# Optimization experiments

Hardware: AMD Instinct MI355X
Metric: run time of the kernel (lower is better)

The kernel has to match this reference:

```python
import jax, jax.numpy as jnp
import numpy as np

TAU = 0.07          # softmax temperature
THR = 0.3           # Jaccard similarity threshold for positive pairs
EPS_NORM = 1e-12    # F.normalize eps


def setup_inputs() -> dict:
    key = jax.random.key(0)
    k1, k2, k3 = jax.random.split(key, 3)
    N, D, A = 4096, 128, 512
    z1 = jax.random.normal(k1, (N, D), dtype=jnp.float32)
    z2 = jax.random.normal(k2, (N, D), dtype=jnp.float32)
    labels = jax.random.randint(k3, (N, A), 0, 2).astype(jnp.int32)
    return {"z1": z1, "z2": z2, "labels": labels}


def _l2_normalize(x):
    n = jnp.linalg.norm(x, axis=-1, keepdims=True)
    return x / jnp.maximum(n, EPS_NORM)


def reference(z1, z2, labels):
    # Implements the N > 1000 (chunked) branch of SupConLoss.forward,
    # vectorized over all anchors at once (chunking is just tiling; math identical).
    N = z1.shape[0]
    idx = jnp.arange(N)

    z1n = _l2_normalize(z1)                       # (N, D)
    z2n = _l2_normalize(z2)                       # (N, D)
    z_all = jnp.concatenate([z1n, z2n], axis=0)   # (2N, D)

    # Jaccard label similarity -> positive-pair mask
    lab = labels.astype(jnp.float32)              # (N, A)
    inter = lab @ lab.T                           # (N, N)
    s = lab.sum(axis=1, keepdims=True)            # (N, 1)
    union = s + s.T - inter
    jaccard = inter / (union + 1e-8)
    pos_label = jaccard >= THR                    # (N, N) bool

    # pos mask over 2N columns: label-positives in both halves,
    # augmented view [j, N+j] forced True, self column [j, j] forced False.
    pos_mask = jnp.concatenate([pos_label, pos_label], axis=1)  # (N, 2N)
    pos_mask = pos_mask.at[idx, N + idx].set(True)
    pos_mask = pos_mask.at[idx, idx].set(False)

    # similarity of z1 anchors against all 2N embeddings
    sim = (z1n @ z_all.T) / TAU                   # (N, 2N)
    sim = sim - jax.lax.stop_gradient(sim.max(axis=1, keepdims=True))
    exp_sim = jnp.exp(sim)

    # denominator excludes the self column [j, j]
    denom = exp_sim.sum(axis=1, keepdims=True) - exp_sim[idx, idx][:, None]
    log_prob = sim - jnp.log(denom + 1e-8)

    num_pos = jnp.maximum(pos_mask.sum(axis=1), 1)
    loss_per_sample = -jnp.where(pos_mask, log_prob, 0.0).sum(axis=1) / num_pos
    return loss_per_sample.sum() / N
```

## Files before the change

### kernel.cpp

```cpp
#include <hip/hip_runtime.h>
#include <math.h>

#define N_ROWS 4096
#define DIM    128
#define A_LAB  512
#define INV_TAU 14.285714285714286f

typedef __attribute__((ext_vector_type(8))) short short8;
typedef __attribute__((ext_vector_type(4))) float f32x4;
typedef __attribute__((ext_vector_type(4))) int i32x4;
typedef __attribute__((ext_vector_type(16))) int i32x16;


__device__ __forceinline__ unsigned short f2bf(float f) {
  unsigned int u = __builtin_bit_cast(unsigned int, f);
  u += 0x7fffu + ((u >> 16) & 1u);
  return (unsigned short)(u >> 16);
}

__device__ __forceinline__ void gl_lds16(const void* g, void* l) {
  __builtin_amdgcn_global_load_lds(
      (const __attribute__((address_space(1))) unsigned int*)g,
      (__attribute__((address_space(3))) unsigned int*)l, 16, 0, 0);
}

__global__ __launch_bounds__(256) void k_norm_pack(
    const float* __restrict__ z1, const float* __restrict__ z2,
    const int* __restrict__ labels,
    unsigned int* __restrict__ zbf, uint2* __restrict__ labs8,
    int* __restrict__ s, float* __restrict__ part, float* __restrict__ out)
{
  {
    const int idx = blockIdx.x * 256 + threadIdx.x;
    if (idx < 3 * 4096) part[idx] = 0.0f;
    if (idx == 0) out[0] = 0.0f;
  }
  const int wave = threadIdx.x >> 6, lane = threadIdx.x & 63;
  const int r = blockIdx.x * 4 + wave;
  const float* src = (r < N_ROWS) ? (z1 + (size_t)r * DIM)
                                  : (z2 + (size_t)(r - N_ROWS) * DIM);
  float2 x = ((const float2*)src)[lane];
  float ss = x.x * x.x + x.y * x.y;
  #pragma unroll
  for (int off = 32; off > 0; off >>= 1) ss += __shfl_xor(ss, off);
  const float inv = 1.0f / fmaxf(sqrtf(ss), 1e-12f);
  const unsigned int lo = f2bf(x.x * inv);
  const unsigned int hi = f2bf(x.y * inv);
  {
    const int U  = lane >> 2;
    const int Up = U ^ (r & 15);
    zbf[(size_t)r * 64 + Up * 4 + (lane & 3)] = (hi << 16) | lo;
  }

  if (r < N_ROWS) {
    const int4* lp = (const int4*)(labels + (size_t)r * A_LAB);
    const int4 a = lp[2 * lane], b = lp[2 * lane + 1];
    const unsigned int w0 = (unsigned int)(a.x != 0)       | ((unsigned int)(a.y != 0) << 8)
                          | ((unsigned int)(a.z != 0) << 16) | ((unsigned int)(a.w != 0) << 24);
    const unsigned int w1 = (unsigned int)(b.x != 0)       | ((unsigned int)(b.y != 0) << 8)
                          | ((unsigned int)(b.z != 0) << 16) | ((unsigned int)(b.w != 0) << 24);
    uint2 v; v.x = w0; v.y = w1;
    const int Ul  = lane >> 1;
    const int cc  = Ul >> 3, uu = Ul & 7;
    const int Ulp = (cc << 3) | (uu ^ (r & 7));
    labs8[(size_t)r * 64 + Ulp * 2 + (lane & 1)] = v;
    int cnt = __popc(w0) + __popc(w1);
    #pragma unroll
    for (int off = 32; off > 0; off >>= 1) cnt += __shfl_xor(cnt, off);
    if (lane == 0) s[r] = cnt;
  }
}

__global__ __launch_bounds__(256, 2) void k_fused(
    const unsigned char* __restrict__ labs8, const int* __restrict__ s,
    const unsigned short* __restrict__ zbf, float* __restrict__ part)
{
  __shared__ uint4 lds[4096];
  __shared__ unsigned int pmL[128 * 4];
  const int tid = threadIdx.x;
  const int ibase = blockIdx.x * 128, jbase = blockIdx.y * 128;
  const int wave = tid >> 6, lane = tid & 63;

  const int jwr = (wave >> 1) * 64, jwc = (wave & 1) * 64;
  const int col32 = lane & 31, h = lane >> 5;

  const int s3i = 3 * s[ibase + jwr + lane];
  const int s3j = 3 * s[jbase + jwc + lane];

  #pragma unroll
  for (int it = 0; it < 4; ++it) {
    const int g = wave * 256 + it * 64 + lane;
    const int r = g >> 3, u = g & 7;
    gl_lds16(labs8 + (((size_t)(ibase + r)) << 9) + u * 16,
             &lds[wave * 256 + it * 64]);
    gl_lds16(labs8 + (((size_t)(jbase + r)) << 9) + u * 16,
             &lds[1024 + wave * 256 + it * 64]);
  }
  __syncthreads();

  i32x16 jacc[2][2];
  #pragma unroll
  for (int rt = 0; rt < 2; ++rt)
    #pragma unroll
    for (int nt = 0; nt < 2; ++nt)
      #pragma unroll
      for (int e = 0; e < 16; ++e) jacc[rt][nt][e] = 0;

  for (int ck = 0; ck < 4; ++ck) {
    const int cur = (ck & 1) * 2048;
    if (ck < 3) {
      const int nxt = ((ck + 1) & 1) * 2048;
      #pragma unroll
      for (int it = 0; it < 4; ++it) {
        const int g = wave * 256 + it * 64 + lane;
        const int r = g >> 3, u = g & 7;
        const size_t go = (size_t)(ck + 1) * 128 + u * 16;
        gl_lds16(labs8 + (((size_t)(ibase + r)) << 9) + go,
                 &lds[nxt + wave * 256 + it * 64]);
        gl_lds16(labs8 + (((size_t)(jbase + r)) << 9) + go,
                 &lds[nxt + 1024 + wave * 256 + it * 64]);
      }
    }
    #pragma unroll
    for (int ks = 0; ks < 4; ++ks) {
      const int u = ks * 2 + h;
      i32x4 a[2], b[2];
      #pragma unroll
      for (int rt = 0; rt < 2; ++rt) {
        const int m = jwr + rt * 32 + col32;
        a[rt] = *(const i32x4*)&lds[cur + m * 8 + (u ^ (m & 7))];
      }
      #pragma unroll
      for (int nt = 0; nt < 2; ++nt) {
        const int m = jwc + nt * 32 + col32;
        b[nt] = *(const i32x4*)&lds[cur + 1024 + m * 8 + (u ^ (m & 7))];
      }
      #pragma unroll
      for (int rt = 0; rt < 2; ++rt)
        #pragma unroll
        for (int nt = 0; nt < 2; ++nt)
          jacc[rt][nt] = __builtin_amdgcn_mfma_i32_32x32x32_i8(a[rt], b[nt], jacc[rt][nt], 0, 0, 0);
    }
    if (ck < 3) __syncthreads();
  }

  __syncthreads();

  {
    const char* gz = (const char*)zbf;
    #pragma unroll
    for (int it = 0; it < 8; ++it) {
      const int g = wave * 512 + it * 64 + lane;
      const int r = g >> 4, u = g & 15;
      gl_lds16(gz + (size_t)(ibase + r) * 256 + u * 16, &lds[wave * 512 + it * 64]);
      gl_lds16(gz + (size_t)(jbase + r) * 256 + u * 16, &lds[2048 + wave * 512 + it * 64]);
    }
  }

  #pragma unroll
  for (int rt = 0; rt < 2; ++rt)
    #pragma unroll
    for (int nt = 0; nt < 2; ++nt) {
      const int wl = (jwc >> 5) + nt;
      const int sj = __shfl(s3j, nt * 32 + col32);
      #pragma unroll
      for (int reg = 0; reg < 16; ++reg) {
        const int r0 = (reg & 3) + 8 * (reg >> 2);
        const int si = __shfl(s3i, rt * 32 + r0 + 4 * h);
        const bool pred = 13 * jacc[rt][nt][reg] >= si + sj;
        const unsigned long long bal = __ballot(pred);
        const int lr = jwr + rt * 32 + r0;
        if (lane == 0)      pmL[lr * 4 + wl]       = (unsigned int)bal;
        else if (lane == 1) pmL[(lr + 4) * 4 + wl] = (unsigned int)(bal >> 32);
      }
    }

  __syncthreads();

  const int col = lane & 15, quad = lane >> 4;
  const int swr = wave * 32;
  const uint4* sAu = lds;
  const uint4* sBu = lds + 2048;

  short8 afr[2][4];
  #pragma unroll
  for (int rt = 0; rt < 2; ++rt)
    #pragma unroll
    for (int kf = 0; kf < 4; ++kf) {
      const int r = swr + rt * 16 + col;
      const int u = kf * 4 + quad;
      afr[rt][kf] = *(const short8*)&sAu[r * 16 + (u ^ (r & 15))];
    }

  float lacc[2][4], Sacc[2][4], Pcnt[2][4];
  #pragma unroll
  for (int rt = 0; rt < 2; ++rt)
    #pragma unroll
    for (int reg = 0; reg < 4; ++reg) { lacc[rt][reg] = 0; Sacc[rt][reg] = 0; Pcnt[rt][reg] = 0; }

  #pragma unroll
  for (int half = 0; half < 2; ++half) {
    f32x4 acc[2][8];
    #pragma unroll
    for (int rt = 0; rt < 2; ++rt)
      #pragma unroll
      for (int nt = 0; nt < 8; ++nt) acc[rt][nt] = (f32x4){0, 0, 0, 0};

    #pragma unroll
    for (int nt = 0; nt < 8; ++nt) {
      short8 bfr[4];
      #pragma unroll
      for (int kf = 0; kf < 4; ++kf) {
        const int r = nt * 16 + col;
        const int u = kf * 4 + quad;
        bfr[kf] = *(const short8*)&sBu[r * 16 + (u ^ (r & 15))];
      }
      #pragma unroll
      for (int rt = 0; rt < 2; ++rt)
        #pragma unroll
        for (int kf = 0; kf < 4; ++kf)
          acc[rt][nt] = __builtin_amdgcn_mfma_f32_16x16x32_bf16(
              afr[rt][kf], bfr[kf], acc[rt][nt], 0, 0, 0);
    }

    if (half == 0) {
      __syncthreads();
      const char* gz = (const char*)zbf;
      #pragma unroll
      for (int it = 0; it < 8; ++it) {
        const int g = wave * 512 + it * 64 + lane;
        const int r = g >> 4, u = g & 15;
        gl_lds16(gz + (size_t)(N_ROWS + jbase + r) * 256 + u * 16,
                 &lds[2048 + wave * 512 + it * 64]);
      }
    }

    const bool left = (half == 0);
    #pragma unroll
    for (int rt = 0; rt < 2; ++rt) {
      unsigned int pw[4][4];
      #pragma unroll
      for (int reg = 0; reg < 4; ++reg) {
        const int li = swr + rt * 16 + quad * 4 + reg;
        #pragma unroll
        for (int w = 0; w < 4; ++w) pw[reg][w] = pmL[li * 4 + w];
      }
      #pragma unroll
      for (int nt = 0; nt < 8; ++nt) {
        const int joff = nt * 16 + col;
        const int jc = jbase + joff;
        const int bitpos = joff & 31;
        const int w = nt >> 1;
        #pragma unroll
        for (int reg = 0; reg < 4; ++reg) {
          const int i = ibase + swr + rt * 16 + quad * 4 + reg;
          const float d = acc[rt][nt][reg];
          const bool bit = (pw[reg][w] >> bitpos) & 1;
          const bool self = left && (jc == i);
          const bool pos = left ? (bit && !self) : (bit || (jc == i));
          const float e = __expf((d - 1.0f) * INV_TAU);
          if (!self) lacc[rt][reg] += e;
          if (pos) { Sacc[rt][reg] += d; Pcnt[rt][reg] += 1.0f; }
        }
      }
    }
    if (half == 0) __syncthreads();
  }

  #pragma unroll
  for (int rt = 0; rt < 2; ++rt)
    #pragma unroll
    for (int reg = 0; reg < 4; ++reg) {
      float l = lacc[rt][reg], S = Sacc[rt][reg], P = Pcnt[rt][reg];
      #pragma unroll
      for (int m = 1; m < 16; m <<= 1) {
        l += __shfl_xor(l, m);
        S += __shfl_xor(S, m);
        P += __shfl_xor(P, m);
      }
      if (col == 0) {
        const int i = ibase + swr + rt * 16 + quad * 4 + reg;
        atomicAdd(&part[i], l);
        atomicAdd(&part[4096 + i], S);
        atomicAdd(&part[8192 + i], P);
      }
    }
}

__global__ __launch_bounds__(128) void k_loss(
    const float* __restrict__ part, float* __restrict__ out)
{
  const int a = blockIdx.x * 128 + threadIdx.x;
  const float l = part[a];
  const float S = part[4096 + a];
  const float P = part[8192 + a];
  const float np = fmaxf(P, 1.0f);
  float v = INV_TAU + logf(l + 1e-8f) - (S * INV_TAU) / np;
  #pragma unroll
  for (int off = 32; off > 0; off >>= 1) v += __shfl_xor(v, off);
  __shared__ float ws2[2];
  const int wave = threadIdx.x >> 6, lane = threadIdx.x & 63;
  if (lane == 0) ws2[wave] = v;
  __syncthreads();
  if (threadIdx.x == 0) atomicAdd(out, (ws2[0] + ws2[1]) * (1.0f / (float)N_ROWS));
}

extern "C" void kernel_launch(void* const* d_in, const int* in_sizes, int n_in,
                              void* d_out, int out_size, void* d_ws, size_t ws_size,
                              hipStream_t stream) {
  const float* z1 = (const float*)d_in[0];
  const float* z2 = (const float*)d_in[1];
  const int* labels = (const int*)d_in[2];
  float* out = (float*)d_out;
  char* ws = (char*)d_ws;

  unsigned int* zbf    = (unsigned int*)(ws);
  uint2* labs8         = (uint2*)(ws + 2097152);
  int* s               = (int*)(ws + 4194304);
  float* part          = (float*)(ws + 4210688);

  hipLaunchKernelGGL(k_norm_pack, dim3(2048), dim3(256), 0, stream,
                     z1, z2, labels, zbf, labs8, s, part, out);
  hipLaunchKernelGGL(k_fused, dim3(32, 32), dim3(256), 0, stream,
                     (const unsigned char*)labs8, s, (const unsigned short*)zbf, part);
  hipLaunchKernelGGL(k_loss, dim3(32), dim3(128), 0, stream, part, out);
}
```

Measured before the change: 111.7 us.

## Halve LDS footprint, load A fragments from global, specialise off-diagonal epilogue

The shared buffer is cut from 64KB to 32KB, which allows a launch bound of 3 blocks per CU. To fit, the label chunks are single-buffered, with a sync and load before every chunk, and the A-side bf16 fragments are read straight from global memory into registers instead of staged in LDS. The epilogue gets a fast path for off-diagonal tiles that skips the self and augmented-view checks, and the exponential becomes a single fma plus exp2. Dropping double buffering exposes label load latency, and the register cap from the tighter launch bound may cause spills.

```diff
diff --git a/kernel.cpp b/kernel.cpp
--- a/kernel.cpp
+++ b/kernel.cpp
@@ -5,6 +5,7 @@
 #define DIM    128
 #define A_LAB  512
 #define INV_TAU 14.285714285714286f
+#define C_EXP   20.609929155556620f
 
 typedef __attribute__((ext_vector_type(8))) short short8;
 typedef __attribute__((ext_vector_type(4))) float f32x4;
@@ -71,15 +72,16 @@
   }
 }
 
-__global__ __launch_bounds__(256, 2) void k_fused(
+__global__ __launch_bounds__(256, 3) void k_fused(
     const unsigned char* __restrict__ labs8, const int* __restrict__ s,
     const unsigned short* __restrict__ zbf, float* __restrict__ part)
 {
-  __shared__ uint4 lds[4096];
+  __shared__ uint4 lds[2048];
   __shared__ unsigned int pmL[128 * 4];
   const int tid = threadIdx.x;
   const int ibase = blockIdx.x * 128, jbase = blockIdx.y * 128;
   const int wave = tid >> 6, lane = tid & 63;
+  const bool diag = (ibase == jbase);
 
   const int jwr = (wave >> 1) * 64, jwc = (wave & 1) * 64;
   const int col32 = lane & 31, h = lane >> 5;
@@ -87,17 +89,6 @@
   const int s3i = 3 * s[ibase + jwr + lane];
   const int s3j = 3 * s[jbase + jwc + lane];
 
-  #pragma unroll
-  for (int it = 0; it < 4; ++it) {
-    const int g = wave * 256 + it * 64 + lane;
-    const int r = g >> 3, u = g & 7;
-    gl_lds16(labs8 + (((size_t)(ibase + r)) << 9) + u * 16,
-             &lds[wave * 256 + it * 64]);
-    gl_lds16(labs8 + (((size_t)(jbase + r)) << 9) + u * 16,
-             &lds[1024 + wave * 256 + it * 64]);
-  }
-  __syncthreads();
-
   i32x16 jacc[2][2];
   #pragma unroll
   for (int rt = 0; rt < 2; ++rt)
@@ -107,20 +98,18 @@
       for (int e = 0; e < 16; ++e) jacc[rt][nt][e] = 0;
 
   for (int ck = 0; ck < 4; ++ck) {
-    const int cur = (ck & 1) * 2048;
-    if (ck < 3) {
-      const int nxt = ((ck + 1) & 1) * 2048;
-      #pragma unroll
-      for (int it = 0; it < 4; ++it) {
-        const int g = wave * 256 + it * 64 + lane;
-        const int r = g >> 3, u = g & 7;
-        const size_t go = (size_t)(ck + 1) * 128 + u * 16;
-        gl_lds16(labs8 + (((size_t)(ibase + r)) << 9) + go,
-                 &lds[nxt + wave * 256 + it * 64]);
-        gl_lds16(labs8 + (((size_t)(jbase + r)) << 9) + go,
-                 &lds[nxt + 1024 + wave * 256 + it * 64]);
-      }
-    }
+    if (ck) __syncthreads();
+    #pragma unroll
+    for (int it = 0; it < 4; ++it) {
+      const int g = wave * 256 + it * 64 + lane;
+      const int r = g >> 3, u = g & 7;
+      const size_t go = (size_t)ck * 128 + u * 16;
+      gl_lds16(labs8 + (((size_t)(ibase + r)) << 9) + go,
+               &lds[wave * 256 + it * 64]);
+      gl_lds16(labs8 + (((size_t)(jbase + r)) << 9) + go,
+               &lds[1024 + wave * 256 + it * 64]);
+    }
+    __syncthreads();
     #pragma unroll
     for (int ks = 0; ks < 4; ++ks) {
       const int u = ks * 2 + h;
@@ -128,12 +117,12 @@
       #pragma unroll
       for (int rt = 0; rt < 2; ++rt) {
         const int m = jwr + rt * 32 + col32;
-        a[rt] = *(const i32x4*)&lds[cur + m * 8 + (u ^ (m & 7))];
+        a[rt] = *(const i32x4*)&lds[m * 8 + (u ^ (m & 7))];
       }
       #pragma unroll
       for (int nt = 0; nt < 2; ++nt) {
         const int m = jwc + nt * 32 + col32;
-        b[nt] = *(const i32x4*)&lds[cur + 1024 + m * 8 + (u ^ (m & 7))];
+        b[nt] = *(const i32x4*)&lds[1024 + m * 8 + (u ^ (m & 7))];
       }
       #pragma unroll
       for (int rt = 0; rt < 2; ++rt)
@@ -141,7 +130,6 @@
         for (int nt = 0; nt < 2; ++nt)
           jacc[rt][nt] = __builtin_amdgcn_mfma_i32_32x32x32_i8(a[rt], b[nt], jacc[rt][nt], 0, 0, 0);
     }
-    if (ck < 3) __syncthreads();
   }
 
   __syncthreads();
@@ -152,9 +140,23 @@
     for (int it = 0; it < 8; ++it) {
       const int g = wave * 512 + it * 64 + lane;
       const int r = g >> 4, u = g & 15;
-      gl_lds16(gz + (size_t)(ibase + r) * 256 + u * 16, &lds[wave * 512 + it * 64]);
-      gl_lds16(gz + (size_t)(jbase + r) * 256 + u * 16, &lds[2048 + wave * 512 + it * 64]);
-    }
+      gl_lds16(gz + (size_t)(jbase + r) * 256 + u * 16, &lds[wave * 512 + it * 64]);
+    }
+  }
+
+  const int col = lane & 15, quad = lane >> 4;
+  const int swr = wave * 32;
+  short8 afr[2][4];
+  {
+    const char* gz = (const char*)zbf;
+    #pragma unroll
+    for (int rt = 0; rt < 2; ++rt)
+      #pragma unroll
+      for (int kf = 0; kf < 4; ++kf) {
+        const int ra = ibase + swr + rt * 16 + col;
+        const int slot = (kf * 4 + quad) ^ (ra & 15);
+        afr[rt][kf] = *(const short8*)(gz + (size_t)ra * 256 + slot * 16);
+      }
   }
 
   #pragma unroll
@@ -177,21 +179,6 @@
 
   __syncthreads();
 
-  const int col = lane & 15, quad = lane >> 4;
-  const int swr = wave * 32;
-  const uint4* sAu = lds;
-  const uint4* sBu = lds + 2048;
-
-  short8 afr[2][4];
-  #pragma unroll
-  for (int rt = 0; rt < 2; ++rt)
-    #pragma unroll
-    for (int kf = 0; kf < 4; ++kf) {
-      const int r = swr + rt * 16 + col;
-      const int u = kf * 4 + quad;
-      afr[rt][kf] = *(const short8*)&sAu[r * 16 + (u ^ (r & 15))];
-    }
-
   float lacc[2][4], Sacc[2][4], Pcnt[2][4];
   #pragma unroll
   for (int rt = 0; rt < 2; ++rt)
@@ -213,7 +200,7 @@
       for (int kf = 0; kf < 4; ++kf) {
         const int r = nt * 16 + col;
         const int u = kf * 4 + quad;
-        bfr[kf] = *(const short8*)&sBu[r * 16 + (u ^ (r & 15))];
+        bfr[kf] = *(const short8*)&lds[r * 16 + (u ^ (r & 15))];
       }
       #pragma unroll
       for (int rt = 0; rt < 2; ++rt)
@@ -231,36 +218,62 @@
         const int g = wave * 512 + it * 64 + lane;
         const int r = g >> 4, u = g & 15;
         gl_lds16(gz + (size_t)(N_ROWS + jbase + r) * 256 + u * 16,
-                 &lds[2048 + wave * 512 + it * 64]);
-      }
-    }
-
-    const bool left = (half == 0);
-    #pragma unroll
-    for (int rt = 0; rt < 2; ++rt) {
-      unsigned int pw[4][4];
-      #pragma unroll
-      for (int reg = 0; reg < 4; ++reg) {
-        const int li = swr + rt * 16 + quad * 4 + reg;
-        #pragma unroll
-        for (int w = 0; w < 4; ++w) pw[reg][w] = pmL[li * 4 + w];
-      }
-      #pragma unroll
-      for (int nt = 0; nt < 8; ++nt) {
-        const int joff = nt * 16 + col;
-        const int jc = jbase + joff;
-        const int bitpos = joff & 31;
-        const int w = nt >> 1;
+                 &lds[wave * 512 + it * 64]);
+      }
+    }
+
+    if (!diag) {
+      #pragma unroll
+      for (int rt = 0; rt < 2; ++rt) {
+        unsigned int pw[4][4];
         #pragma unroll
         for (int reg = 0; reg < 4; ++reg) {
-          const int i = ibase + swr + rt * 16 + quad * 4 + reg;
-          const float d = acc[rt][nt][reg];
-          const bool bit = (pw[reg][w] >> bitpos) & 1;
-          const bool self = left && (jc == i);
-          const bool pos = left ? (bit && !self) : (bit || (jc == i));
-          const float e = __expf((d - 1.0f) * INV_TAU);
-          if (!self) lacc[rt][reg] += e;
-          if (pos) { Sacc[rt][reg] += d; Pcnt[rt][reg] += 1.0f; }
+          const int li = swr + rt * 16 + quad * 4 + reg;
+          #pragma unroll
+          for (int w = 0; w < 4; ++w) pw[reg][w] = pmL[li * 4 + w];
+        }
+        #pragma unroll
+        for (int nt = 0; nt < 8; ++nt) {
+          const int joff = nt * 16 + col;
+          const int bitpos = joff & 31;
+          const int w = nt >> 1;
+          #pragma unroll
+          for (int reg = 0; reg < 4; ++reg) {
+            const float d = acc[rt][nt][reg];
+            const bool bit = (pw[reg][w] >> bitpos) & 1;
+            lacc[rt][reg] += exp2f(fmaf(d, C_EXP, -C_EXP));
+            if (bit) { Sacc[rt][reg] += d; Pcnt[rt][reg] += 1.0f; }
+          }
+        }
+      }
+    } else {
+      const bool left = (half == 0);
+      #pragma unroll
+      for (int rt = 0; rt < 2; ++rt) {
+        unsigned int pw[4][4];
+        #pragma unroll
+        for (int reg = 0; reg < 4; ++reg) {
+          const int li = swr + rt * 16 + quad * 4 + reg;
+          #pragma unroll
+          for (int w = 0; w < 4; ++w) pw[reg][w] = pmL[li * 4 + w];
+        }
+        #pragma unroll
+        for (int nt = 0; nt < 8; ++nt) {
+          const int joff = nt * 16 + col;
+          const int jc = jbase + joff;
+          const int bitpos = joff & 31;
+          const int w = nt >> 1;
+          #pragma unroll
+          for (int reg = 0; reg < 4; ++reg) {
+            const int i = ibase + swr + rt * 16 + quad * 4 + reg;
+            const float d = acc[rt][nt][reg];
+            const bool bit = (pw[reg][w] >> bitpos) & 1;
+            const bool self = left && (jc == i);
+            const bool pos = left ? (bit && !self) : (bit || (jc == i));
+            const float e = exp2f(fmaf(d, C_EXP, -C_EXP));
+            if (!self) lacc[rt][reg] += e;
+            if (pos) { Sacc[rt][reg] += d; Pcnt[rt][reg] += 1.0f; }
+          }
         }
       }
     }
```

Result: faster. 109.4 us (-2.1%).
